# Kernel tuning notes

Hardware: AMD Instinct MI355X
Metric: run time of the kernel (lower is better)

The kernel has to match this reference:

```python
import jax, jax.numpy as jnp
import numpy as np

B, C, H, W = 2, 128, 256, 256
HEADS, SH, SW = 8, 8, 8
SHIFT, TOPK = 4, 16
N = SH * SW  # tokens per window = 64
SCALE = (C // HEADS) ** -0.5


def _rel_index():
    # torch.meshgrid default is 'ij' indexing
    hh, ww = np.meshgrid(np.arange(SH), np.arange(SW), indexing='ij')
    cf = np.stack([hh.ravel(), ww.ravel()])            # [2, N]
    rel = cf[:, :, None] - cf[:, None, :]              # [2, N, N]
    return (rel[0] + SH - 1) * (2 * SW - 1) + (rel[1] + SW - 1)  # [N, N]


def setup_inputs() -> dict:
    key = jax.random.key(0)
    k1, k2, k3, k4 = jax.random.split(key, 4)
    return {
        'query': jax.random.normal(k1, (B, C, H, W), jnp.float32),
        'key': jax.random.normal(k2, (B, C, H, W), jnp.float32),
        'value': jax.random.normal(k3, (B, C, H, W), jnp.float32),
        'rel_pos_table': 0.02 * jax.random.normal(k4, ((2 * SH - 1) * (2 * SW - 1), HEADS), jnp.float32),
    }


def _part(x):
    # 'b (k c) (n h) (m w) -> (b n m) k (h w) c'
    n, m, c = H // SH, W // SW, C // HEADS
    x = x.reshape(B, HEADS, c, n, SH, m, SW)
    return x.transpose(0, 3, 5, 1, 4, 6, 2).reshape(B * n * m, HEADS, N, c)


def reference(query, key, value, rel_pos_table):
    n, m, c = H // SH, W // SW, C // HEADS
    # base_view='left', shift>0: zero leftmost SHIFT columns, roll k/v right
    mask = jnp.ones((B, H, W), query.dtype).at[:, :, :SHIFT].set(0.0)
    key = jnp.roll(key, SHIFT, axis=-1)
    value = jnp.roll(value, SHIFT, axis=-1)
    q = _part(query) * SCALE
    k = _part(key)
    v = _part(value)
    # 'b (n s) (m q) -> (b n m) (s q)' then view(-1,1,1,N)
    mask = mask.reshape(B, n, SH, m, SW).transpose(0, 1, 3, 2, 4).reshape(B * n * m, 1, 1, N)
    attn = jnp.einsum('bhqc,bhkc->bhqk', q, k)  # [B*n*m, heads, N, N]
    idx = jax.lax.top_k(attn, TOPK)[1]
    knn_mask = jnp.put_along_axis(jnp.zeros_like(attn), idx, 1.0, axis=-1, inplace=False)
    ridx = jnp.asarray(_rel_index())
    bias = rel_pos_table[ridx.reshape(-1)].reshape(N, N, HEADS).transpose(2, 0, 1)[None]
    attn = jax.nn.softmax(attn + bias, axis=-1) * mask * knn_mask
    out = jnp.einsum('bhqk,bhkc->bhqc', attn, v)  # [B*n*m, heads, N, c]
    # '(b n m) k (h w) c -> b (k c) (n h) (m w)'
    out = out.reshape(B, n, m, HEADS, SH, SW, c).transpose(0, 3, 6, 1, 4, 2, 5).reshape(B, C, H, W)
    return out
```

## Files before the change

kernel.cpp:

```cpp
#include <hip/hip_runtime.h>

#define HW_ (256 * 256)

__global__ __launch_bounds__(256, 4)
void slice_attn_kernel(const float* __restrict__ Q,
                       const float* __restrict__ K,
                       const float* __restrict__ V,
                       const float* __restrict__ RT,
                       float* __restrict__ O) {
  __shared__ __align__(16) float k_lds[4][1024];
  __shared__ __align__(16) float v_lds[4][1024];
  __shared__ float bias_lds[225];

  const int tid  = threadIdx.x;
  const int wave = tid >> 6;
  const int t    = tid & 63;
  const int bid  = blockIdx.x;

  const int wm = ((bid & 7) << 2) | wave;
  const int wn = (bid >> 3) & 31;
  const int h  = (bid >> 8) & 7;
  const int b  = bid >> 11;

  if (tid < 225) bias_lds[tid] = RT[tid * 8 + h];

  const int sh = t >> 3, sw = t & 7;
  const int y  = wn * 8 + sh;
  const int x  = wm * 8 + sw;
  const int xs = (x - 4) & 255;

  const int base = (b * 128 + h * 16) * HW_;
  const float* qp = Q + base + y * 256 + x;
  const float* kp = K + base + y * 256 + xs;
  const float* vp = V + base + y * 256 + xs;

  float* kl = k_lds[wave];
  float* vl = v_lds[wave];

  float qr[16];
  #pragma unroll
  for (int c4 = 0; c4 < 4; ++c4) {
    float4 kv, vv;
    kv.x = kp[(c4 * 4 + 0) * HW_];
    kv.y = kp[(c4 * 4 + 1) * HW_];
    kv.z = kp[(c4 * 4 + 2) * HW_];
    kv.w = kp[(c4 * 4 + 3) * HW_];
    vv.x = vp[(c4 * 4 + 0) * HW_];
    vv.y = vp[(c4 * 4 + 1) * HW_];
    vv.z = vp[(c4 * 4 + 2) * HW_];
    vv.w = vp[(c4 * 4 + 3) * HW_];
    *reinterpret_cast<float4*>(kl + t * 16 + c4 * 4) = kv;
    *reinterpret_cast<float4*>(vl + t * 16 + c4 * 4) = vv;
    qr[c4 * 4 + 0] = qp[(c4 * 4 + 0) * HW_] * 0.25f;
    qr[c4 * 4 + 1] = qp[(c4 * 4 + 1) * HW_] * 0.25f;
    qr[c4 * 4 + 2] = qp[(c4 * 4 + 2) * HW_] * 0.25f;
    qr[c4 * 4 + 3] = qp[(c4 * 4 + 3) * HW_] * 0.25f;
  }
  __syncthreads();

  float s[64];
  {
    #pragma clang fp contract(off)
    #pragma unroll
    for (int kt = 0; kt < 64; ++kt) {
      const float4* kr = reinterpret_cast<const float4*>(kl + kt * 16);
      const float4 k0 = kr[0], k1 = kr[1], k2 = kr[2], k3 = kr[3];
      const float p0  = qr[0]  * k0.x;
      const float p1  = qr[1]  * k0.y;
      const float p2  = qr[2]  * k0.z;
      const float p3  = qr[3]  * k0.w;
      const float p4  = qr[4]  * k1.x;
      const float p5  = qr[5]  * k1.y;
      const float p6  = qr[6]  * k1.z;
      const float p7  = qr[7]  * k1.w;
      const float p8  = qr[8]  * k2.x;
      const float p9  = qr[9]  * k2.y;
      const float p10 = qr[10] * k2.z;
      const float p11 = qr[11] * k2.w;
      const float p12 = qr[12] * k3.x;
      const float p13 = qr[13] * k3.y;
      const float p14 = qr[14] * k3.z;
      const float p15 = qr[15] * k3.w;
      const float L0 = ((p0 + p4) + p8)  + p12;
      const float L1 = ((p1 + p5) + p9)  + p13;
      const float L2 = ((p2 + p6) + p10) + p14;
      const float L3 = ((p3 + p7) + p11) + p15;
      s[kt] = (L0 + L1) + (L2 + L3);
    }
  }

  #pragma unroll 1
  for (int r = 0; r < 16; ++r) {
    float tmp[32];
    #pragma unroll
    for (int i = 0; i < 32; ++i) tmp[i] = fmaxf(s[i], s[i + 32]);
    #pragma unroll
    for (int wdt = 16; wdt >= 1; wdt >>= 1) {
      #pragma unroll
      for (int i = 0; i < wdt; ++i) tmp[i] = fmaxf(tmp[i], tmp[i + wdt]);
    }
    const float mv  = tmp[0];
    const float kv2 = mv - 1024.0f;
    bool taken = false;
    #pragma unroll
    for (int i = 0; i < 64; ++i) {
      const bool hit = (!taken) && (s[i] == mv);
      s[i] = hit ? kv2 : s[i];
      taken = taken || hit;
    }
  }

  const int vbase = sh * 15 + sw;
  const float* bp = &bias_lds[vbase];
  unsigned selLo = 0u, selHi = 0u;
  #pragma unroll
  for (int i = 0; i < 64; ++i) {
    const float bv  = bp[112 - (i >> 3) * 15 - (i & 7)];
    const bool sel  = s[i] < -512.0f;
    const float orig = sel ? s[i] + 1024.0f : s[i];
    s[i] = orig + bv;
    if (i < 32) selLo |= sel ? (1u << i) : 0u;
    else        selHi |= sel ? (1u << (i - 32)) : 0u;
  }

  {
    float tmp[32];
    #pragma unroll
    for (int i = 0; i < 32; ++i) tmp[i] = fmaxf(s[i], s[i + 32]);
    #pragma unroll
    for (int wdt = 16; wdt >= 1; wdt >>= 1) {
      #pragma unroll
      for (int i = 0; i < wdt; ++i) tmp[i] = fmaxf(tmp[i], tmp[i + wdt]);
    }
    const float m = tmp[0];
    float d0 = 0.f, d1 = 0.f, d2 = 0.f, d3 = 0.f;
    #pragma unroll
    for (int i = 0; i < 64; i += 4) {
      const float p0 = __expf(s[i] - m);
      const float p1 = __expf(s[i + 1] - m);
      const float p2 = __expf(s[i + 2] - m);
      const float p3 = __expf(s[i + 3] - m);
      s[i] = p0; s[i + 1] = p1; s[i + 2] = p2; s[i + 3] = p3;
      d0 += p0; d1 += p1; d2 += p2; d3 += p3;
    }
    const float denom = (d0 + d1) + (d2 + d3);
    const float inv = 1.0f / denom;
    const bool edge = (wm == 0);
    #pragma unroll
    for (int i = 0; i < 64; ++i) {
      const unsigned bit = (i < 32) ? (selLo >> i) : (selHi >> (i - 32));
      float w = (bit & 1u) ? s[i] * inv : 0.0f;
      if (edge && (i & 7) < 4) w = 0.0f;
      s[i] = w;
    }
  }

  float acc[16];
  #pragma unroll
  for (int cc = 0; cc < 16; ++cc) acc[cc] = 0.0f;
  #pragma unroll
  for (int kt = 0; kt < 64; ++kt) {
    const float w = s[kt];
    const float4* vr = reinterpret_cast<const float4*>(vl + kt * 16);
    const float4 v0 = vr[0], v1 = vr[1], v2 = vr[2], v3 = vr[3];
    acc[0]  += w * v0.x; acc[1]  += w * v0.y; acc[2]  += w * v0.z; acc[3]  += w * v0.w;
    acc[4]  += w * v1.x; acc[5]  += w * v1.y; acc[6]  += w * v1.z; acc[7]  += w * v1.w;
    acc[8]  += w * v2.x; acc[9]  += w * v2.y; acc[10] += w * v2.z; acc[11] += w * v2.w;
    acc[12] += w * v3.x; acc[13] += w * v3.y; acc[14] += w * v3.z; acc[15] += w * v3.w;
  }

  float* op = O + base + y * 256 + x;
  #pragma unroll
  for (int cc = 0; cc < 16; ++cc) op[cc * HW_] = acc[cc];
}

extern "C" void kernel_launch(void* const* d_in, const int* in_sizes, int n_in,
                              void* d_out, int out_size, void* d_ws, size_t ws_size,
                              hipStream_t stream) {
  const float* Q  = (const float*)d_in[0];
  const float* K  = (const float*)d_in[1];
  const float* V  = (const float*)d_in[2];
  const float* RT = (const float*)d_in[3];
  float* O = (float*)d_out;
  dim3 grid(4096), block(256);
  hipLaunchKernelGGL(slice_attn_kernel, grid, block, 0, stream, Q, K, V, RT, O);
}
```

Baseline: 212.2 us.

## Replace iterative top-k argmax with bitonic sort threshold selection

Replaces the 16-round max-and-mark top-k loop with a full in-register bitonic sort of the 64 scores. The 16th-largest value becomes a threshold, and a single counting pass builds the selection bitmask, taking earlier indices first on ties. The softmax max now comes from the sorted array and the bias is added inside the exp loop, which relies on softmax being shift-invariant. Launch bounds drop to 2 blocks per CU to give the extra 64-float sort array more registers, which may lower occupancy.

```diff
diff --git a/kernel.cpp b/kernel.cpp
--- a/kernel.cpp
+++ b/kernel.cpp
@@ -2,7 +2,7 @@
 
 #define HW_ (256 * 256)
 
-__global__ __launch_bounds__(256, 4)
+__global__ __launch_bounds__(256, 2)
 void slice_attn_kernel(const float* __restrict__ Q,
                        const float* __restrict__ K,
                        const float* __restrict__ V,
@@ -89,57 +89,59 @@
     }
   }
 
-  #pragma unroll 1
-  for (int r = 0; r < 16; ++r) {
-    float tmp[32];
+  float c[64];
+  #pragma unroll
+  for (int i = 0; i < 64; ++i) c[i] = s[i];
+  #pragma unroll
+  for (int k = 2; k <= 64; k <<= 1) {
     #pragma unroll
-    for (int i = 0; i < 32; ++i) tmp[i] = fmaxf(s[i], s[i + 32]);
-    #pragma unroll
-    for (int wdt = 16; wdt >= 1; wdt >>= 1) {
+    for (int j = k >> 1; j > 0; j >>= 1) {
       #pragma unroll
-      for (int i = 0; i < wdt; ++i) tmp[i] = fmaxf(tmp[i], tmp[i + wdt]);
+      for (int i = 0; i < 64; ++i) {
+        const int l = i ^ j;
+        if (l > i) {
+          const bool up = ((i & k) == 0);
+          const float a = c[i], bb = c[l];
+          const float mn = fminf(a, bb), mx = fmaxf(a, bb);
+          c[i] = up ? mn : mx;
+          c[l] = up ? mx : mn;
+        }
+      }
     }
-    const float mv  = tmp[0];
-    const float kv2 = mv - 1024.0f;
-    bool taken = false;
+  }
+  const float thr = c[48];
+  const float m   = c[63];
+
+  int cgt = 0;
+  #pragma unroll
+  for (int i = 0; i < 64; ++i) cgt += (s[i] > thr) ? 1 : 0;
+  unsigned selLo = 0u, selHi = 0u;
+  {
+    int cnt = cgt;
     #pragma unroll
     for (int i = 0; i < 64; ++i) {
-      const bool hit = (!taken) && (s[i] == mv);
-      s[i] = hit ? kv2 : s[i];
-      taken = taken || hit;
+      const bool eq   = (s[i] == thr);
+      const bool take = (s[i] > thr) || (eq && (cnt < 16));
+      cnt += eq ? 1 : 0;
+      if (i < 32) selLo |= take ? (1u << i) : 0u;
+      else        selHi |= take ? (1u << (i - 32)) : 0u;
     }
   }
 
   const int vbase = sh * 15 + sw;
   const float* bp = &bias_lds[vbase];
-  unsigned selLo = 0u, selHi = 0u;
-  #pragma unroll
-  for (int i = 0; i < 64; ++i) {
-    const float bv  = bp[112 - (i >> 3) * 15 - (i & 7)];
-    const bool sel  = s[i] < -512.0f;
-    const float orig = sel ? s[i] + 1024.0f : s[i];
-    s[i] = orig + bv;
-    if (i < 32) selLo |= sel ? (1u << i) : 0u;
-    else        selHi |= sel ? (1u << (i - 32)) : 0u;
-  }
-
   {
-    float tmp[32];
-    #pragma unroll
-    for (int i = 0; i < 32; ++i) tmp[i] = fmaxf(s[i], s[i + 32]);
-    #pragma unroll
-    for (int wdt = 16; wdt >= 1; wdt >>= 1) {
-      #pragma unroll
-      for (int i = 0; i < wdt; ++i) tmp[i] = fmaxf(tmp[i], tmp[i + wdt]);
-    }
-    const float m = tmp[0];
     float d0 = 0.f, d1 = 0.f, d2 = 0.f, d3 = 0.f;
     #pragma unroll
     for (int i = 0; i < 64; i += 4) {
-      const float p0 = __expf(s[i] - m);
-      const float p1 = __expf(s[i + 1] - m);
-      const float p2 = __expf(s[i + 2] - m);
-      const float p3 = __expf(s[i + 3] - m);
+      const float b0 = bp[112 - ((i + 0) >> 3) * 15 - ((i + 0) & 7)];
+      const float b1 = bp[112 - ((i + 1) >> 3) * 15 - ((i + 1) & 7)];
+      const float b2 = bp[112 - ((i + 2) >> 3) * 15 - ((i + 2) & 7)];
+      const float b3 = bp[112 - ((i + 3) >> 3) * 15 - ((i + 3) & 7)];
+      const float p0 = __expf(s[i + 0] + b0 - m);
+      const float p1 = __expf(s[i + 1] + b1 - m);
+      const float p2 = __expf(s[i + 2] + b2 - m);
+      const float p3 = __expf(s[i + 3] + b3 - m);
       s[i] = p0; s[i + 1] = p1; s[i + 2] = p2; s[i + 3] = p3;
       d0 += p0; d1 += p1; d2 += p2; d3 += p3;
     }
```

Result: faster. 200.4 us (-5.5%).

## Split each query row across four lanes with shuffle-based top-k and fused softmax

Applied to the files above, without the earlier changes.

Each block now handles a single window and head, with its K/V tile shared by all four waves. Each query row is split across four lanes that each own 16 keys. Top-k selection uses cross-lane max shuffles plus a ballot for tie-breaking, and the softmax, masking and PV product are fused into one loop. Partial sums are combined with xor shuffles, and each lane writes four output channels. The aim is to cut per-thread registers (16 scores instead of 64) and the K/V LDS footprint, raising occupancy and parallelism. The cost is four times more blocks, redundant Q loads across lanes, and shuffle traffic inside every top-k iteration.

```diff
diff --git a/kernel.cpp b/kernel.cpp
--- a/kernel.cpp
+++ b/kernel.cpp
@@ -8,63 +8,66 @@
                        const float* __restrict__ V,
                        const float* __restrict__ RT,
                        float* __restrict__ O) {
-  __shared__ __align__(16) float k_lds[4][1024];
-  __shared__ __align__(16) float v_lds[4][1024];
+  __shared__ __align__(16) float k_lds[1024];
+  __shared__ __align__(16) float v_lds[1024];
   __shared__ float bias_lds[225];
 
   const int tid  = threadIdx.x;
   const int wave = tid >> 6;
-  const int t    = tid & 63;
-  const int bid  = blockIdx.x;
+  const int lane = tid & 63;
+  const int r    = lane & 15;
+  const int q    = lane >> 4;
+  const int row  = wave * 16 + r;
 
-  const int wm = ((bid & 7) << 2) | wave;
-  const int wn = (bid >> 3) & 31;
-  const int h  = (bid >> 8) & 7;
-  const int b  = bid >> 11;
+  const int unit = blockIdx.x;
+  const int wm = unit & 31;
+  const int wn = (unit >> 5) & 31;
+  const int h  = (unit >> 10) & 7;
+  const int b  = unit >> 13;
 
   if (tid < 225) bias_lds[tid] = RT[tid * 8 + h];
 
-  const int sh = t >> 3, sw = t & 7;
-  const int y  = wn * 8 + sh;
-  const int x  = wm * 8 + sw;
-  const int xs = (x - 4) & 255;
+  const int base = (b * 128 + h * 16) * HW_;
 
-  const int base = (b * 128 + h * 16) * HW_;
+  {
+    const int key = tid & 63;
+    const int c4g = tid >> 6;
+    const int kh = key >> 3, kw = key & 7;
+    const int yk = wn * 8 + kh;
+    const int xk = (wm * 8 + kw - 4) & 255;
+    const float* kp = K + base + yk * 256 + xk;
+    const float* vp = V + base + yk * 256 + xk;
+    float4 kv, vv;
+    kv.x = kp[(c4g * 4 + 0) * HW_];
+    kv.y = kp[(c4g * 4 + 1) * HW_];
+    kv.z = kp[(c4g * 4 + 2) * HW_];
+    kv.w = kp[(c4g * 4 + 3) * HW_];
+    vv.x = vp[(c4g * 4 + 0) * HW_];
+    vv.y = vp[(c4g * 4 + 1) * HW_];
+    vv.z = vp[(c4g * 4 + 2) * HW_];
+    vv.w = vp[(c4g * 4 + 3) * HW_];
+    *reinterpret_cast<float4*>(k_lds + c4g * 256 + key * 4) = kv;
+    *reinterpret_cast<float4*>(v_lds + c4g * 256 + key * 4) = vv;
+  }
+
+  const int sh = row >> 3, sw = row & 7;
+  const int y = wn * 8 + sh, x = wm * 8 + sw;
   const float* qp = Q + base + y * 256 + x;
-  const float* kp = K + base + y * 256 + xs;
-  const float* vp = V + base + y * 256 + xs;
-
-  float* kl = k_lds[wave];
-  float* vl = v_lds[wave];
-
   float qr[16];
   #pragma unroll
-  for (int c4 = 0; c4 < 4; ++c4) {
-    float4 kv, vv;
-    kv.x = kp[(c4 * 4 + 0) * HW_];
-    kv.y = kp[(c4 * 4 + 1) * HW_];
-    kv.z = kp[(c4 * 4 + 2) * HW_];
-    kv.w = kp[(c4 * 4 + 3) * HW_];
-    vv.x = vp[(c4 * 4 + 0) * HW_];
-    vv.y = vp[(c4 * 4 + 1) * HW_];
-    vv.z = vp[(c4 * 4 + 2) * HW_];
-    vv.w = vp[(c4 * 4 + 3) * HW_];
-    *reinterpret_cast<float4*>(kl + t * 16 + c4 * 4) = kv;
-    *reinterpret_cast<float4*>(vl + t * 16 + c4 * 4) = vv;
-    qr[c4 * 4 + 0] = qp[(c4 * 4 + 0) * HW_] * 0.25f;
-    qr[c4 * 4 + 1] = qp[(c4 * 4 + 1) * HW_] * 0.25f;
-    qr[c4 * 4 + 2] = qp[(c4 * 4 + 2) * HW_] * 0.25f;
-    qr[c4 * 4 + 3] = qp[(c4 * 4 + 3) * HW_] * 0.25f;
-  }
+  for (int i = 0; i < 16; ++i) qr[i] = qp[i * HW_] * 0.25f;
   __syncthreads();
 
-  float s[64];
+  float s[16];
   {
     #pragma clang fp contract(off)
     #pragma unroll
-    for (int kt = 0; kt < 64; ++kt) {
-      const float4* kr = reinterpret_cast<const float4*>(kl + kt * 16);
-      const float4 k0 = kr[0], k1 = kr[1], k2 = kr[2], k3 = kr[3];
+    for (int j = 0; j < 16; ++j) {
+      const int kt = q * 16 + j;
+      const float4 k0 = *reinterpret_cast<const float4*>(k_lds + 0 * 256 + kt * 4);
+      const float4 k1 = *reinterpret_cast<const float4*>(k_lds + 1 * 256 + kt * 4);
+      const float4 k2 = *reinterpret_cast<const float4*>(k_lds + 2 * 256 + kt * 4);
+      const float4 k3 = *reinterpret_cast<const float4*>(k_lds + 3 * 256 + kt * 4);
       const float p0  = qr[0]  * k0.x;
       const float p1  = qr[1]  * k0.y;
       const float p2  = qr[2]  * k0.z;
@@ -85,93 +88,91 @@
       const float L1 = ((p1 + p5) + p9)  + p13;
       const float L2 = ((p2 + p6) + p10) + p14;
       const float L3 = ((p3 + p7) + p11) + p15;
-      s[kt] = (L0 + L1) + (L2 + L3);
+      s[j] = (L0 + L1) + (L2 + L3);
     }
   }
 
+  const unsigned long long bitp = 1ull << lane;
+  const unsigned long long lmask =
+      (q > 0 ? (1ull << r) : 0ull) |
+      (q > 1 ? (1ull << (16 + r)) : 0ull) |
+      (q > 2 ? (1ull << (32 + r)) : 0ull);
+  (void)bitp;
+
+  float m = 0.0f;
   #pragma unroll 1
-  for (int r = 0; r < 16; ++r) {
-    float tmp[32];
+  for (int rr = 0; rr < 16; ++rr) {
+    float t8[8];
     #pragma unroll
-    for (int i = 0; i < 32; ++i) tmp[i] = fmaxf(s[i], s[i + 32]);
+    for (int i = 0; i < 8; ++i) t8[i] = fmaxf(s[i], s[i + 8]);
     #pragma unroll
-    for (int wdt = 16; wdt >= 1; wdt >>= 1) {
+    for (int wdt = 4; wdt >= 1; wdt >>= 1) {
       #pragma unroll
-      for (int i = 0; i < wdt; ++i) tmp[i] = fmaxf(tmp[i], tmp[i + wdt]);
+      for (int i = 0; i < wdt; ++i) t8[i] = fmaxf(t8[i], t8[i + wdt]);
     }
-    const float mv  = tmp[0];
+    const float own = t8[0];
+    float mv = fmaxf(own, __shfl_xor(own, 16));
+    mv = fmaxf(mv, __shfl_xor(mv, 32));
+    if (rr == 0) m = mv;
+    const bool has = (own == mv);
+    const unsigned long long bal = __ballot(has);
+    bool taken = (bal & lmask) != 0ull;
     const float kv2 = mv - 1024.0f;
-    bool taken = false;
     #pragma unroll
-    for (int i = 0; i < 64; ++i) {
-      const bool hit = (!taken) && (s[i] == mv);
-      s[i] = hit ? kv2 : s[i];
+    for (int j = 0; j < 16; ++j) {
+      const bool hit = (!taken) && (s[j] == mv);
+      s[j] = hit ? kv2 : s[j];
       taken = taken || hit;
     }
   }
 
   const int vbase = sh * 15 + sw;
   const float* bp = &bias_lds[vbase];
-  unsigned selLo = 0u, selHi = 0u;
-  #pragma unroll
-  for (int i = 0; i < 64; ++i) {
-    const float bv  = bp[112 - (i >> 3) * 15 - (i & 7)];
-    const bool sel  = s[i] < -512.0f;
-    const float orig = sel ? s[i] + 1024.0f : s[i];
-    s[i] = orig + bv;
-    if (i < 32) selLo |= sel ? (1u << i) : 0u;
-    else        selHi |= sel ? (1u << (i - 32)) : 0u;
-  }
-
-  {
-    float tmp[32];
-    #pragma unroll
-    for (int i = 0; i < 32; ++i) tmp[i] = fmaxf(s[i], s[i + 32]);
-    #pragma unroll
-    for (int wdt = 16; wdt >= 1; wdt >>= 1) {
-      #pragma unroll
-      for (int i = 0; i < wdt; ++i) tmp[i] = fmaxf(tmp[i], tmp[i + wdt]);
-    }
-    const float m = tmp[0];
-    float d0 = 0.f, d1 = 0.f, d2 = 0.f, d3 = 0.f;
-    #pragma unroll
-    for (int i = 0; i < 64; i += 4) {
-      const float p0 = __expf(s[i] - m);
-      const float p1 = __expf(s[i + 1] - m);
-      const float p2 = __expf(s[i + 2] - m);
-      const float p3 = __expf(s[i + 3] - m);
-      s[i] = p0; s[i + 1] = p1; s[i + 2] = p2; s[i + 3] = p3;
-      d0 += p0; d1 += p1; d2 += p2; d3 += p3;
-    }
-    const float denom = (d0 + d1) + (d2 + d3);
-    const float inv = 1.0f / denom;
-    const bool edge = (wm == 0);
-    #pragma unroll
-    for (int i = 0; i < 64; ++i) {
-      const unsigned bit = (i < 32) ? (selLo >> i) : (selHi >> (i - 32));
-      float w = (bit & 1u) ? s[i] * inv : 0.0f;
-      if (edge && (i & 7) < 4) w = 0.0f;
-      s[i] = w;
-    }
-  }
+  const bool edge = (wm == 0);
 
   float acc[16];
   #pragma unroll
-  for (int cc = 0; cc < 16; ++cc) acc[cc] = 0.0f;
+  for (int j = 0; j < 16; ++j) acc[j] = 0.0f;
+  float d0 = 0.0f, d1 = 0.0f;
   #pragma unroll
-  for (int kt = 0; kt < 64; ++kt) {
-    const float w = s[kt];
-    const float4* vr = reinterpret_cast<const float4*>(vl + kt * 16);
-    const float4 v0 = vr[0], v1 = vr[1], v2 = vr[2], v3 = vr[3];
-    acc[0]  += w * v0.x; acc[1]  += w * v0.y; acc[2]  += w * v0.z; acc[3]  += w * v0.w;
-    acc[4]  += w * v1.x; acc[5]  += w * v1.y; acc[6]  += w * v1.z; acc[7]  += w * v1.w;
-    acc[8]  += w * v2.x; acc[9]  += w * v2.y; acc[10] += w * v2.z; acc[11] += w * v2.w;
-    acc[12] += w * v3.x; acc[13] += w * v3.y; acc[14] += w * v3.z; acc[15] += w * v3.w;
+  for (int j = 0; j < 16; ++j) {
+    const int ig = q * 16 + j;
+    const float sv = s[j];
+    const bool sel = sv < -512.0f;
+    const float orig = sel ? sv + 1024.0f : sv;
+    const float bv = bp[112 - (ig >> 3) * 15 - (ig & 7)];
+    const float p  = __expf(orig + bv - m);
+    if (j & 1) d1 += p; else d0 += p;
+    float w = sel ? p : 0.0f;
+    if (edge && (ig & 7) < 4) w = 0.0f;
+    const float4 vq0 = *reinterpret_cast<const float4*>(v_lds + 0 * 256 + ig * 4);
+    const float4 vq1 = *reinterpret_cast<const float4*>(v_lds + 1 * 256 + ig * 4);
+    const float4 vq2 = *reinterpret_cast<const float4*>(v_lds + 2 * 256 + ig * 4);
+    const float4 vq3 = *reinterpret_cast<const float4*>(v_lds + 3 * 256 + ig * 4);
+    acc[0]  += w * vq0.x; acc[1]  += w * vq0.y; acc[2]  += w * vq0.z; acc[3]  += w * vq0.w;
+    acc[4]  += w * vq1.x; acc[5]  += w * vq1.y; acc[6]  += w * vq1.z; acc[7]  += w * vq1.w;
+    acc[8]  += w * vq2.x; acc[9]  += w * vq2.y; acc[10] += w * vq2.z; acc[11] += w * vq2.w;
+    acc[12] += w * vq3.x; acc[13] += w * vq3.y; acc[14] += w * vq3.z; acc[15] += w * vq3.w;
   }
 
-  float* op = O + base + y * 256 + x;
+  float d = d0 + d1;
+  d += __shfl_xor(d, 16);
+  d += __shfl_xor(d, 32);
+  const float inv = 1.0f / d;
   #pragma unroll
-  for (int cc = 0; cc < 16; ++cc) op[cc * HW_] = acc[cc];
+  for (int j = 0; j < 16; ++j) {
+    acc[j] += __shfl_xor(acc[j], 16);
+    acc[j] += __shfl_xor(acc[j], 32);
+  }
+
+  float* op = O + base + y * 256 + x + (q * 4) * HW_;
+  #pragma unroll
+  for (int jj = 0; jj < 4; ++jj) {
+    const float s01 = (q & 1) ? acc[4 + jj]  : acc[jj];
+    const float s23 = (q & 1) ? acc[12 + jj] : acc[8 + jj];
+    const float val = (q & 2) ? s23 : s01;
+    op[jj * HW_] = val * inv;
+  }
 }
 
 extern "C" void kernel_launch(void* const* d_in, const int* in_sizes, int n_in,
@@ -182,6 +183,6 @@
   const float* V  = (const float*)d_in[2];
   const float* RT = (const float*)d_in[3];
   float* O = (float*)d_out;
-  dim3 grid(4096), block(256);
+  dim3 grid(16384), block(256);
   hipLaunchKernelGGL(slice_attn_kernel, grid, block, 0, stream, Q, K, V, RT, O);
 }
```

Result: slower. 304.0 us (+43.3%).
